# Performance work log

Measured on AMD Instinct MI355X. Metric: run time of the kernel, lower is better.

The kernel has to match this reference:

```python
import jax, jax.numpy as jnp
import numpy as np
from jax import lax

B, IT, Z, Y, X = 1, 10, 192, 192, 192
DX = 20.0


def _shift_zero(x, axis, off):
    # out[i] = x[i + off] where valid, zero elsewhere (matches torch _shift_zero)
    n = x.shape[axis]
    pad = [(0, 0)] * x.ndim
    if off > 0:
        pad[axis] = (0, off)
        xp = jnp.pad(x, pad)
        return lax.slice_in_dim(xp, off, off + n, axis=axis)
    else:
        pad[axis] = (-off, 0)
        xp = jnp.pad(x, pad)
        return lax.slice_in_dim(xp, 0, n, axis=axis)


def _stencil25_laplacian(x, dx):
    dx2 = dx * dx
    c0 = -205.0 / 72.0 / dx2
    coeffs = (8.0 / 5.0 / dx2, -1.0 / 5.0 / dx2, 8.0 / 315.0 / dx2, -1.0 / 560.0 / dx2)
    lap = (c0 * 3.0) * x
    for d, c in enumerate(coeffs, start=1):
        taps = (_shift_zero(x, 1, -d) + _shift_zero(x, 1, d)
                + _shift_zero(x, 2, -d) + _shift_zero(x, 2, d)
                + _shift_zero(x, 3, -d) + _shift_zero(x, 3, d))
        lap = lap + c * taps
    return lap


def run_25pt_stencil(vp, source_terms, dx):
    # source_terms: [B, T, Z, Y, X] -> scan over T
    src_t = jnp.moveaxis(source_terms, 1, 0)  # [T, B, Z, Y, X]

    def step(carry, s_t):
        prev, cur = carry
        upd = 2.0 * cur - prev + vp * _stencil25_laplacian(cur, dx) + s_t
        return (cur, upd), None

    zero = jnp.zeros_like(vp)
    (_, current), _ = lax.scan(step, (zero, zero), src_t)
    return current


def setup_inputs() -> dict:
    key = jax.random.key(0)
    k1, k2, k3 = jax.random.split(key, 3)
    vp = jax.random.uniform(k1, (B, Z, Y, X), dtype=jnp.float32) * 4.0
    source_terms = jax.random.normal(k2, (B, IT, Z, Y, X), dtype=jnp.float32)
    ref = jax.random.normal(k3, (B, Z, Y, X), dtype=jnp.float32)
    return {"vp": vp, "source_terms": source_terms, "ref": ref}


def reference(vp, source_terms, ref):
    output = run_25pt_stencil(vp, source_terms, DX)
    error = (output - ref).astype(jnp.float32)
    loss = jnp.mean(error * error)
    max_abs_error = jnp.max(jnp.abs(error))
    return (loss, output, max_abs_error)
```

## Files before the change

### kernel.cpp

```cpp
#include <hip/hip_runtime.h>

#define NX   192
#define NXY  (192 * 192)
#define N3   (192 * 192 * 192)
#define ZCHUNK 24

constexpr double DX2 = 400.0;
#define C0 ((float)(-205.0 / 72.0 / DX2 * 3.0))
#define C1 ((float)(8.0 / 5.0 / DX2))
#define C2 ((float)(-1.0 / 5.0 / DX2))
#define C3 ((float)(8.0 / 315.0 / DX2))
#define C4 ((float)(-1.0 / 560.0 / DX2))

template <int MODE>
__global__ __launch_bounds__(256)
void step_kernel(const float* __restrict__ cur,
                 const float* __restrict__ prev,
                 const float* __restrict__ vp,
                 const float* __restrict__ src,
                 float* __restrict__ out,
                 const float* __restrict__ ref,
                 double* __restrict__ loss_sum,
                 unsigned int* __restrict__ max_bits)
{
    const int tx = threadIdx.x;
    const int ty = threadIdx.y;
    const int x  = blockIdx.x * 64 + tx;
    const int y  = blockIdx.y * 4 + ty;
    const int z0 = blockIdx.z * ZCHUNK;

    const bool vxm1 = x >= 1, vxm2 = x >= 2, vxm3 = x >= 3, vxm4 = x >= 4;
    const bool vxp1 = x < NX - 1, vxp2 = x < NX - 2, vxp3 = x < NX - 3, vxp4 = x < NX - 4;
    const bool vym1 = y >= 1, vym2 = y >= 2, vym3 = y >= 3, vym4 = y >= 4;
    const bool vyp1 = y < NX - 1, vyp2 = y < NX - 2, vyp3 = y < NX - 3, vyp4 = y < NX - 4;

    const float* curcol = cur + (size_t)y * NX + x;

    auto ldz = [&](int z) -> float {
        return (z >= 0 && z < NX) ? curcol[(size_t)z * NXY] : 0.0f;
    };
    float w0 = ldz(z0 - 4);
    float w1 = ldz(z0 - 3);
    float w2 = ldz(z0 - 2);
    float w3 = ldz(z0 - 1);
    float w4 = ldz(z0 + 0);
    float w5 = ldz(z0 + 1);
    float w6 = ldz(z0 + 2);
    float w7 = ldz(z0 + 3);
    float w8;

    float facc = 0.0f;
    float fmax = 0.0f;

    size_t idx = (size_t)z0 * NXY + (size_t)y * NX + x;

    #pragma unroll 4
    for (int z = z0; z < z0 + ZCHUNK; ++z) {
        w8 = (z + 4 < NX) ? curcol[(size_t)(z + 4) * NXY] : 0.0f;

        const float* cp = cur + idx;
        const float center = w4;

        float t1 = (w3 + w5);
        t1 += (vym1 ? cp[-1 * NX] : 0.0f);
        t1 += (vyp1 ? cp[ 1 * NX] : 0.0f);
        t1 += (vxm1 ? cp[-1] : 0.0f);
        t1 += (vxp1 ? cp[ 1] : 0.0f);

        float t2 = (w2 + w6);
        t2 += (vym2 ? cp[-2 * NX] : 0.0f);
        t2 += (vyp2 ? cp[ 2 * NX] : 0.0f);
        t2 += (vxm2 ? cp[-2] : 0.0f);
        t2 += (vxp2 ? cp[ 2] : 0.0f);

        float t3 = (w1 + w7);
        t3 += (vym3 ? cp[-3 * NX] : 0.0f);
        t3 += (vyp3 ? cp[ 3 * NX] : 0.0f);
        t3 += (vxm3 ? cp[-3] : 0.0f);
        t3 += (vxp3 ? cp[ 3] : 0.0f);

        float t4 = (w0 + w8);
        t4 += (vym4 ? cp[-4 * NX] : 0.0f);
        t4 += (vyp4 ? cp[ 4 * NX] : 0.0f);
        t4 += (vxm4 ? cp[-4] : 0.0f);
        t4 += (vxp4 ? cp[ 4] : 0.0f);

        float lap = C0 * center;
        lap += C1 * t1;
        lap += C2 * t2;
        lap += C3 * t3;
        lap += C4 * t4;

        float prevv;
        if constexpr (MODE == 0) prevv = 0.0f;
        else                     prevv = prev[idx];

        const float v = vp[idx];
        const float s = src[idx];
        const float upd = ((2.0f * center - prevv) + v * lap) + s;
        out[idx] = upd;

        if constexpr (MODE == 2) {
            const float err = upd - ref[idx];
            facc += err * err;
            fmax = fmaxf(fmax, fabsf(err));
        }

        w0 = w1; w1 = w2; w2 = w3; w3 = w4;
        w4 = w5; w5 = w6; w6 = w7; w7 = w8;
        idx += NXY;
    }

    if constexpr (MODE == 2) {
        double s = (double)facc;
        float  m = fmax;
        #pragma unroll
        for (int off = 32; off > 0; off >>= 1) {
            s += __shfl_down(s, off);
            m = fmaxf(m, __shfl_down(m, off));
        }
        __shared__ double sred[4];
        __shared__ float  mred[4];
        const int tid  = ty * 64 + tx;
        const int lane = tid & 63;
        const int wv   = tid >> 6;
        if (lane == 0) { sred[wv] = s; mred[wv] = m; }
        __syncthreads();
        if (tid == 0) {
            double st = (sred[0] + sred[1]) + (sred[2] + sred[3]);
            float  mt = fmaxf(fmaxf(mred[0], mred[1]), fmaxf(mred[2], mred[3]));
            atomicAdd(loss_sum, st);
            atomicMax(max_bits, __float_as_uint(mt));
        }
    }
}

__global__ void init_accum(double* loss_sum, unsigned int* max_bits)
{
    *loss_sum = 0.0;
    *max_bits = 0u;
}

__global__ void finalize_kernel(const double* loss_sum, const unsigned int* max_bits,
                                float* out)
{
    out[0]      = (float)(*loss_sum / (double)N3);
    out[N3 + 1] = __uint_as_float(*max_bits);
}

extern "C" void kernel_launch(void* const* d_in, const int* in_sizes, int n_in,
                              void* d_out, int out_size, void* d_ws, size_t ws_size,
                              hipStream_t stream)
{
    const float* vp     = (const float*)d_in[0];
    const float* srcall = (const float*)d_in[1];
    const float* ref    = (const float*)d_in[2];

    float* out = (float*)d_out;
    float* A   = out + 1;
    float* B   = (float*)d_ws;

    double*       lsum  = (double*)((char*)d_ws + (size_t)N3 * sizeof(float));
    unsigned int* mbits = (unsigned int*)(lsum + 1);

    const dim3 blk(64, 4, 1);
    const dim3 grd(NX / 64, NX / 4, NX / ZCHUNK);

    init_accum<<<1, 1, 0, stream>>>(lsum, mbits);

    step_kernel<0><<<grd, blk, 0, stream>>>(srcall, nullptr, vp, srcall + (size_t)1 * N3,
                                            A, nullptr, nullptr, nullptr);
    step_kernel<1><<<grd, blk, 0, stream>>>(A, srcall, vp, srcall + (size_t)2 * N3,
                                            B, nullptr, nullptr, nullptr);
    const float* cur = B;  const float* prv = A;  float* dst = A;
    for (int t = 3; t <= 8; ++t) {
        step_kernel<1><<<grd, blk, 0, stream>>>(cur, prv, vp, srcall + (size_t)t * N3,
                                                dst, nullptr, nullptr, nullptr);
        const float* ncur = dst;
        dst = (float*)cur;
        prv = cur;
        cur = ncur;
    }
    step_kernel<2><<<grd, blk, 0, stream>>>(cur, prv, vp, srcall + (size_t)9 * N3,
                                            (float*)dst, ref, lsum, mbits);

    finalize_kernel<<<1, 1, 0, stream>>>(lsum, mbits, out);
}
```

Measured before the change: 748.8 us.

## Vectorize stencil to four x-points per thread with float4 loads

Each thread now computes four consecutive x outputs using 128-bit vector loads. The x-direction taps come from the centre vector plus left and right neighbour vectors instead of eight scalar loads. The block shape changes to 16x16 covering 64x16 in x-y, and the z chunk shrinks from 24 to 8 to keep enough blocks for parallelism. This cuts load instruction count and redundant x-neighbour loads, but raises per-thread register use and the share of z-halo reloads per chunk.

```diff
diff --git a/kernel.cpp b/kernel.cpp
--- a/kernel.cpp
+++ b/kernel.cpp
@@ -3,7 +3,9 @@
 #define NX   192
 #define NXY  (192 * 192)
 #define N3   (192 * 192 * 192)
-#define ZCHUNK 24
+#define ZCHUNK 8
+
+typedef float f4 __attribute__((ext_vector_type(4)));
 
 constexpr double DX2 = 400.0;
 #define C0 ((float)(-205.0 / 72.0 / DX2 * 3.0))
@@ -11,6 +13,8 @@
 #define C2 ((float)(-1.0 / 5.0 / DX2))
 #define C3 ((float)(8.0 / 315.0 / DX2))
 #define C4 ((float)(-1.0 / 560.0 / DX2))
+
+#define AT(j) ((j) < 4 ? L[(j)] : ((j) < 8 ? C[(j) - 4] : R[(j) - 8]))
 
 template <int MODE>
 __global__ __launch_bounds__(256)
@@ -25,85 +29,89 @@
 {
     const int tx = threadIdx.x;
     const int ty = threadIdx.y;
-    const int x  = blockIdx.x * 64 + tx;
-    const int y  = blockIdx.y * 4 + ty;
+    const int x0 = blockIdx.x * 64 + tx * 4;
+    const int y  = blockIdx.y * 16 + ty;
     const int z0 = blockIdx.z * ZCHUNK;
 
-    const bool vxm1 = x >= 1, vxm2 = x >= 2, vxm3 = x >= 3, vxm4 = x >= 4;
-    const bool vxp1 = x < NX - 1, vxp2 = x < NX - 2, vxp3 = x < NX - 3, vxp4 = x < NX - 4;
+    const f4 zf4 = {0.0f, 0.0f, 0.0f, 0.0f};
+
+    const bool lvalid = (x0 != 0);
+    const bool rvalid = (x0 != NX - 4);
+
     const bool vym1 = y >= 1, vym2 = y >= 2, vym3 = y >= 3, vym4 = y >= 4;
     const bool vyp1 = y < NX - 1, vyp2 = y < NX - 2, vyp3 = y < NX - 3, vyp4 = y < NX - 4;
 
-    const float* curcol = cur + (size_t)y * NX + x;
+    const float* curcol = cur + (size_t)y * NX + x0;
 
-    auto ldz = [&](int z) -> float {
-        return (z >= 0 && z < NX) ? curcol[(size_t)z * NXY] : 0.0f;
+    auto ldz = [&](int zz) -> f4 {
+        return (zz >= 0 && zz < NX) ? *(const f4*)(curcol + (size_t)zz * NXY) : zf4;
     };
-    float w0 = ldz(z0 - 4);
-    float w1 = ldz(z0 - 3);
-    float w2 = ldz(z0 - 2);
-    float w3 = ldz(z0 - 1);
-    float w4 = ldz(z0 + 0);
-    float w5 = ldz(z0 + 1);
-    float w6 = ldz(z0 + 2);
-    float w7 = ldz(z0 + 3);
-    float w8;
+
+    f4 w0 = ldz(z0 - 4), w1 = ldz(z0 - 3), w2 = ldz(z0 - 2), w3 = ldz(z0 - 1);
+    f4 w4 = ldz(z0), w5 = ldz(z0 + 1), w6 = ldz(z0 + 2), w7 = ldz(z0 + 3);
+    f4 w8;
 
     float facc = 0.0f;
     float fmax = 0.0f;
 
-    size_t idx = (size_t)z0 * NXY + (size_t)y * NX + x;
+    size_t idx = (size_t)z0 * NXY + (size_t)y * NX + x0;
 
-    #pragma unroll 4
     for (int z = z0; z < z0 + ZCHUNK; ++z) {
-        w8 = (z + 4 < NX) ? curcol[(size_t)(z + 4) * NXY] : 0.0f;
+        w8 = (z + 4 < NX) ? *(const f4*)(curcol + (size_t)(z + 4) * NXY) : zf4;
 
         const float* cp = cur + idx;
-        const float center = w4;
 
-        float t1 = (w3 + w5);
-        t1 += (vym1 ? cp[-1 * NX] : 0.0f);
-        t1 += (vyp1 ? cp[ 1 * NX] : 0.0f);
-        t1 += (vxm1 ? cp[-1] : 0.0f);
-        t1 += (vxp1 ? cp[ 1] : 0.0f);
+        const f4 ym1 = vym1 ? *(const f4*)(cp - 1 * NX) : zf4;
+        const f4 yp1 = vyp1 ? *(const f4*)(cp + 1 * NX) : zf4;
+        const f4 ym2 = vym2 ? *(const f4*)(cp - 2 * NX) : zf4;
+        const f4 yp2 = vyp2 ? *(const f4*)(cp + 2 * NX) : zf4;
+        const f4 ym3 = vym3 ? *(const f4*)(cp - 3 * NX) : zf4;
+        const f4 yp3 = vyp3 ? *(const f4*)(cp + 3 * NX) : zf4;
+        const f4 ym4 = vym4 ? *(const f4*)(cp - 4 * NX) : zf4;
+        const f4 yp4 = vyp4 ? *(const f4*)(cp + 4 * NX) : zf4;
 
-        float t2 = (w2 + w6);
-        t2 += (vym2 ? cp[-2 * NX] : 0.0f);
-        t2 += (vyp2 ? cp[ 2 * NX] : 0.0f);
-        t2 += (vxm2 ? cp[-2] : 0.0f);
-        t2 += (vxp2 ? cp[ 2] : 0.0f);
+        const f4 L = lvalid ? *(const f4*)(cp - 4) : zf4;
+        const f4 R = rvalid ? *(const f4*)(cp + 4) : zf4;
+        const f4 C = w4;
 
-        float t3 = (w1 + w7);
-        t3 += (vym3 ? cp[-3 * NX] : 0.0f);
-        t3 += (vyp3 ? cp[ 3 * NX] : 0.0f);
-        t3 += (vxm3 ? cp[-3] : 0.0f);
-        t3 += (vxp3 ? cp[ 3] : 0.0f);
+        const f4 t1v = ((w3 + w5) + ym1) + yp1;
+        const f4 t2v = ((w2 + w6) + ym2) + yp2;
+        const f4 t3v = ((w1 + w7) + ym3) + yp3;
+        const f4 t4v = ((w0 + w8) + ym4) + yp4;
 
-        float t4 = (w0 + w8);
-        t4 += (vym4 ? cp[-4 * NX] : 0.0f);
-        t4 += (vyp4 ? cp[ 4 * NX] : 0.0f);
-        t4 += (vxm4 ? cp[-4] : 0.0f);
-        t4 += (vxp4 ? cp[ 4] : 0.0f);
+        const f4 vpv = *(const f4*)(vp + idx);
+        const f4 sv  = *(const f4*)(src + idx);
+        f4 pv;
+        if constexpr (MODE == 0) pv = zf4;
+        else                     pv = *(const f4*)(prev + idx);
 
-        float lap = C0 * center;
-        lap += C1 * t1;
-        lap += C2 * t2;
-        lap += C3 * t3;
-        lap += C4 * t4;
+        f4 upd;
+        #pragma unroll
+        for (int i = 0; i < 4; ++i) {
+            const float t1 = (t1v[i] + AT(4 + i - 1)) + AT(4 + i + 1);
+            const float t2 = (t2v[i] + AT(4 + i - 2)) + AT(4 + i + 2);
+            const float t3 = (t3v[i] + AT(4 + i - 3)) + AT(4 + i + 3);
+            const float t4 = (t4v[i] + AT(4 + i - 4)) + AT(4 + i + 4);
 
-        float prevv;
-        if constexpr (MODE == 0) prevv = 0.0f;
-        else                     prevv = prev[idx];
+            float lap = C0 * C[i];
+            lap += C1 * t1;
+            lap += C2 * t2;
+            lap += C3 * t3;
+            lap += C4 * t4;
 
-        const float v = vp[idx];
-        const float s = src[idx];
-        const float upd = ((2.0f * center - prevv) + v * lap) + s;
-        out[idx] = upd;
+            upd[i] = ((2.0f * C[i] - pv[i]) + vpv[i] * lap) + sv[i];
+        }
+
+        *(f4*)(out + idx) = upd;
 
         if constexpr (MODE == 2) {
-            const float err = upd - ref[idx];
-            facc += err * err;
-            fmax = fmaxf(fmax, fabsf(err));
+            const f4 rv = *(const f4*)(ref + idx);
+            #pragma unroll
+            for (int i = 0; i < 4; ++i) {
+                const float err = upd[i] - rv[i];
+                facc += err * err;
+                fmax = fmaxf(fmax, fabsf(err));
+            }
         }
 
         w0 = w1; w1 = w2; w2 = w3; w3 = w4;
@@ -121,7 +129,7 @@
         }
         __shared__ double sred[4];
         __shared__ float  mred[4];
-        const int tid  = ty * 64 + tx;
+        const int tid  = threadIdx.y * 16 + threadIdx.x;
         const int lane = tid & 63;
         const int wv   = tid >> 6;
         if (lane == 0) { sred[wv] = s; mred[wv] = m; }
@@ -163,8 +171,8 @@
     double*       lsum  = (double*)((char*)d_ws + (size_t)N3 * sizeof(float));
     unsigned int* mbits = (unsigned int*)(lsum + 1);
 
-    const dim3 blk(64, 4, 1);
-    const dim3 grd(NX / 64, NX / 4, NX / ZCHUNK);
+    const dim3 blk(16, 16, 1);
+    const dim3 grd(NX / 64, NX / 16, NX / ZCHUNK);
 
     init_accum<<<1, 1, 0, stream>>>(lsum, mbits);
 
```

Result: faster. 719.5 us (-3.9%).
